# Kernel optimization log

Hardware: AMD Instinct MI355X
Metric: run time of the kernel (lower is better)

## Reference

```python
import jax, jax.numpy as jnp
import numpy as np

D_MODEL = 1024
NUM_HEADS = 16
D_FF = 4096
MAX_SEQ_LEN = 2048
THETA = 10000.0
EPS = 1e-5
B, S = 2, 2048


def setup_inputs() -> dict:
    key = jax.random.key(0)
    ks = jax.random.split(key, 10)
    scale = 0.02
    inp = {
        "in_features": jax.random.normal(ks[0], (B, S, D_MODEL), dtype=jnp.float32),
        "token_positions": jnp.broadcast_to(jnp.arange(S, dtype=jnp.int32), (B, S)),
        "q_w": jax.random.normal(ks[1], (D_MODEL, D_MODEL), dtype=jnp.float32) * scale,
        "k_w": jax.random.normal(ks[2], (D_MODEL, D_MODEL), dtype=jnp.float32) * scale,
        "v_w": jax.random.normal(ks[3], (D_MODEL, D_MODEL), dtype=jnp.float32) * scale,
        "o_w": jax.random.normal(ks[4], (D_MODEL, D_MODEL), dtype=jnp.float32) * scale,
        "ln1_w": jnp.ones((D_MODEL,), dtype=jnp.float32),
        "ln2_w": jnp.ones((D_MODEL,), dtype=jnp.float32),
        "ffn_w1": jax.random.normal(ks[5], (D_FF, D_MODEL), dtype=jnp.float32) * scale,
        "ffn_w2": jax.random.normal(ks[6], (D_MODEL, D_FF), dtype=jnp.float32) * scale,
        "ffn_w3": jax.random.normal(ks[7], (D_FF, D_MODEL), dtype=jnp.float32) * scale,
    }
    return inp


def _rmsnorm(x, w, eps=EPS):
    return x * jax.lax.rsqrt(jnp.mean(x * x, axis=-1, keepdims=True) + eps) * w


def _rope(x, pos, theta=THETA):
    # x: [B, H, S, Dh]; pos: [B, S] int
    dh = x.shape[-1]
    inv_freq = theta ** (-jnp.arange(0, dh, 2, dtype=jnp.float32) / dh)  # [Dh/2]
    ang = pos.astype(jnp.float32)[..., None] * inv_freq                  # [B, S, Dh/2]
    cos = jnp.cos(ang)[:, None, :, :]  # [B, 1, S, Dh/2]
    sin = jnp.sin(ang)[:, None, :, :]
    x1, x2 = x[..., 0::2], x[..., 1::2]
    r1 = x1 * cos - x2 * sin
    r2 = x1 * sin + x2 * cos
    return jnp.stack([r1, r2], axis=-1).reshape(x.shape)


def _block(x, pos, q_w, k_w, v_w, o_w, ln1_w, ln2_w, w1, w2, w3):
    b, s, d = x.shape
    h, dh = NUM_HEADS, d // NUM_HEADS
    # Pre-LN attention
    xn = _rmsnorm(x, ln1_w)
    q = jnp.einsum('bsd,ed->bse', xn, q_w).reshape(b, s, h, dh).transpose(0, 2, 1, 3)
    k = jnp.einsum('bsd,ed->bse', xn, k_w).reshape(b, s, h, dh).transpose(0, 2, 1, 3)
    v = jnp.einsum('bsd,ed->bse', xn, v_w).reshape(b, s, h, dh).transpose(0, 2, 1, 3)
    q = _rope(q, pos)
    k = _rope(k, pos)
    scores = jnp.einsum('bhqd,bhkd->bhqk', q, k) / jnp.sqrt(jnp.float32(dh))
    causal = jnp.tril(jnp.ones((s, s), dtype=bool))
    scores = jnp.where(causal, scores, jnp.float32(-1e9))
    attn = jax.nn.softmax(scores, axis=-1)
    ctx = jnp.einsum('bhqk,bhkd->bhqd', attn, v).transpose(0, 2, 1, 3).reshape(b, s, d)
    attn_out = jnp.einsum('bsd,ed->bse', ctx, o_w)
    x = x + attn_out
    # Pre-LN SwiGLU FFN
    xn2 = _rmsnorm(x, ln2_w)
    g = jnp.einsum('bsd,fd->bsf', xn2, w1)
    u = jnp.einsum('bsd,fd->bsf', xn2, w3)
    ffn_out = jnp.einsum('bsf,df->bsd', jax.nn.silu(g) * u, w2)
    return x + ffn_out


def reference(in_features, token_positions, q_w, k_w, v_w, o_w, ln1_w, ln2_w, ffn_w1, ffn_w2, ffn_w3):
    return _block(in_features, token_positions, q_w, k_w, v_w, o_w, ln1_w, ln2_w, ffn_w1, ffn_w2, ffn_w3)
```

## Files before the change

### kernel.cpp

```cpp
#include <hip/hip_runtime.h>
#include <hip/hip_bf16.h>

typedef __attribute__((ext_vector_type(8))) __bf16 bf16x8;
typedef __attribute__((ext_vector_type(4))) float f32x4;

#define DEV static __device__ __forceinline__

DEV unsigned short f2bf(float f) {
  __bf16 h = (__bf16)f;
  union { __bf16 h; unsigned short u; } v; v.h = h;
  return v.u;
}
DEV float bf2f(unsigned short h) {
  union { unsigned int u; float f; } v; v.u = ((unsigned int)h) << 16;
  return v.f;
}
DEV f32x4 mfma16(bf16x8 a, bf16x8 b, f32x4 c) {
  return __builtin_amdgcn_mfma_f32_16x16x32_bf16(a, b, c, 0, 0, 0);
}
DEV void gload_lds16(const void* g, void* l) {
  __builtin_amdgcn_global_load_lds((__attribute__((address_space(1))) void*)g,
                                   (__attribute__((address_space(3))) void*)l,
                                   16, 0, 0);
}
#if __has_builtin(__builtin_amdgcn_exp2f)
DEV float fexp2(float x) { return __builtin_amdgcn_exp2f(x); }
#else
DEV float fexp2(float x) { return exp2f(x); }
#endif

struct CvtArgs { const float* src[7]; int cum[8]; };
__global__ __launch_bounds__(256) void cvt_all(CvtArgs a, unsigned short* __restrict__ dst) {
  int i = (blockIdx.x * 256 + threadIdx.x) * 4;
  if (i >= a.cum[7]) return;
  int w = 0;
#pragma unroll 7
  for (int t = 0; t < 7; ++t) if (i >= a.cum[t + 1]) w = t + 1;
  float4 v = *(const float4*)(a.src[w] + (i - a.cum[w]));
  dst[i + 0] = f2bf(v.x);
  dst[i + 1] = f2bf(v.y);
  dst[i + 2] = f2bf(v.z);
  dst[i + 3] = f2bf(v.w);
}

__global__ __launch_bounds__(256) void rmsnorm_k(const float* __restrict__ x,
                                                 const float* __restrict__ w,
                                                 unsigned short* __restrict__ out) {
  int row = blockIdx.x;
  int tid = threadIdx.x;
  const float* xr = x + (size_t)row * 1024;
  float4 v = *(const float4*)(xr + tid * 4);
  float ss = v.x * v.x + v.y * v.y + v.z * v.z + v.w * v.w;
#pragma unroll
  for (int m = 32; m >= 1; m >>= 1) ss += __shfl_xor(ss, m);
  __shared__ float red[4];
  int wid = tid >> 6;
  if ((tid & 63) == 0) red[wid] = ss;
  __syncthreads();
  float tot = red[0] + red[1] + red[2] + red[3];
  float rs = rsqrtf(tot * (1.0f / 1024.0f) + 1e-5f);
  float4 wv = *(const float4*)(w + tid * 4);
  unsigned short* o = out + (size_t)row * 1024 + tid * 4;
  o[0] = f2bf(v.x * rs * wv.x);
  o[1] = f2bf(v.y * rs * wv.y);
  o[2] = f2bf(v.z * rs * wv.z);
  o[3] = f2bf(v.w * rs * wv.w);
}

__global__ __launch_bounds__(256) void rope2_k(unsigned short* __restrict__ q,
                                               unsigned short* __restrict__ k,
                                               const int* __restrict__ pos) {
  int gid = blockIdx.x * 256 + threadIdx.x;
  unsigned short* x = (gid < 2097152) ? q : k;
  int idx = gid & 2097151;
  int i = idx & 31;
  int s = (idx >> 5) & 2047;
  int bh = idx >> 16;
  int b = bh >> 4;
  float p = (float)pos[b * 2048 + s];
  float inv = exp2f(-(float)i * 0.4152410118609203f);
  float ang = p * inv;
  float sn = sinf(ang), cs = cosf(ang);
  size_t base = (((size_t)bh * 2048) + s) * 64 + 2 * i;
  float x1 = bf2f(x[base]), x2 = bf2f(x[base + 1]);
  x[base]     = f2bf(x1 * cs - x2 * sn);
  x[base + 1] = f2bf(x1 * sn + x2 * cs);
}

template <int MODE>
DEV void gemm8_body(const unsigned short* __restrict__ A, int lda,
                    const unsigned short* __restrict__ B, int ldb,
                    int bm, int bn, int kbase, int nt,
                    unsigned short* __restrict__ outb, float* __restrict__ outf,
                    const float* __restrict__ resid, const unsigned short* __restrict__ gate,
                    unsigned short* As, unsigned short* Bs) {
  const int tid = threadIdx.x;
  const int lane = tid & 63, wid = tid >> 6;
  const int wr = wid >> 2, wc = wid & 3;
  const int m0 = bm * 256, n0 = bn * 256;

  const int r0 = tid >> 2, r1 = 128 + (tid >> 2), cc = tid & 3;
  const int sc0 = (cc ^ ((r0 >> 1) & 3)) * 8;
  const int sc1 = (cc ^ ((r1 >> 1) & 3)) * 8;
  const size_t arow0 = (size_t)(m0 + r0) * lda, arow1 = (size_t)(m0 + r1) * lda;
  const size_t brow0 = (size_t)(n0 + r0) * ldb, brow1 = (size_t)(n0 + r1) * ldb;
  const int du0 = tid * 8, du1 = (512 + tid) * 8;

  auto stA = [&](int t, int kh) {
    unsigned short* d = As + ((((t & 1) << 1) | kh) * 8192);
    const unsigned short* s = A + kbase + t * 64 + kh * 32;
    gload_lds16(s + arow0 + sc0, d + du0);
    gload_lds16(s + arow1 + sc1, d + du1);
  };
  auto stB = [&](int t, int kh) {
    unsigned short* d = Bs + ((((t & 1) << 1) | kh) * 8192);
    const unsigned short* s = B + kbase + t * 64 + kh * 32;
    gload_lds16(s + brow0 + sc0, d + du0);
    gload_lds16(s + brow1 + sc1, d + du1);
  };

  const int fcol = ((lane >> 4) ^ ((lane >> 1) & 3)) * 8;
  const int frow = lane & 15;
  const int abase = (wr * 128 + frow) * 32 + fcol;
  const int bbase = (wc * 64 + frow) * 32 + fcol;

  f32x4 acc[8][4] = {};
  bf16x8 a[4], b[4];

#define LOADA(buf, ks, mh) { const unsigned short* p_ = As + (((buf) << 1) | (ks)) * 8192 + abase + (mh) * 2048; \
  a[0] = *(const bf16x8*)(p_); a[1] = *(const bf16x8*)(p_ + 512); \
  a[2] = *(const bf16x8*)(p_ + 1024); a[3] = *(const bf16x8*)(p_ + 1536); }
#define LOADB(buf, ks) { const unsigned short* p_ = Bs + (((buf) << 1) | (ks)) * 8192 + bbase; \
  b[0] = *(const bf16x8*)(p_); b[1] = *(const bf16x8*)(p_ + 512); \
  b[2] = *(const bf16x8*)(p_ + 1024); b[3] = *(const bf16x8*)(p_ + 1536); }
#define MFMAQ(mh) { _Pragma("unroll") for (int fi = 0; fi < 4; ++fi) \
  _Pragma("unroll") for (int j = 0; j < 4; ++j) \
    acc[(mh) * 4 + fi][j] = mfma16(a[fi], b[j], acc[(mh) * 4 + fi][j]); }
#define LGK0() { asm volatile("s_waitcnt lgkmcnt(0)" ::: "memory"); __builtin_amdgcn_sched_barrier(0); }

  stA(0, 0); stB(0, 0); stA(0, 1); stB(0, 1);
  stA(1, 0); stB(1, 0);
  asm volatile("s_waitcnt vmcnt(4)" ::: "memory");
  __builtin_amdgcn_s_barrier();

  for (int t = 0; t < nt; ++t) {
    const int buf = t & 1;
    LOADA(buf, 0, 0); LOADB(buf, 0);
    if (t + 1 < nt) stA(t + 1, 1);
    __builtin_amdgcn_s_barrier();
    LGK0();
    __builtin_amdgcn_s_setprio(1); MFMAQ(0); __builtin_amdgcn_s_setprio(0);
    __builtin_amdgcn_s_barrier();
    LOADA(buf, 0, 1);
    if (t + 1 < nt) stB(t + 1, 1);
    __builtin_amdgcn_s_barrier();
    LGK0();
    __builtin_amdgcn_s_setprio(1); MFMAQ(1); __builtin_amdgcn_s_setprio(0);
    __builtin_amdgcn_s_barrier();
    LOADA(buf, 1, 0); LOADB(buf, 1);
    if (t + 2 < nt) stA(t + 2, 0);
    __builtin_amdgcn_s_barrier();
    LGK0();
    __builtin_amdgcn_s_setprio(1); MFMAQ(0); __builtin_amdgcn_s_setprio(0);
    __builtin_amdgcn_s_barrier();
    LOADA(buf, 1, 1);
    if (t + 2 < nt) stB(t + 2, 0);
    __builtin_amdgcn_s_barrier();
    LGK0();
    __builtin_amdgcn_s_setprio(1); MFMAQ(1); __builtin_amdgcn_s_setprio(0);
    if (t + 1 < nt) {
      if (t + 2 < nt) { asm volatile("s_waitcnt vmcnt(4)" ::: "memory"); }
      else            { asm volatile("s_waitcnt vmcnt(0)" ::: "memory"); }
      __builtin_amdgcn_s_barrier();
    }
  }
#undef LOADA
#undef LOADB
#undef MFMAQ
#undef LGK0

#pragma unroll
  for (int i = 0; i < 8; ++i)
#pragma unroll
    for (int j = 0; j < 4; ++j)
#pragma unroll
      for (int r = 0; r < 4; ++r) {
        int m = m0 + wr * 128 + i * 16 + ((lane >> 4) << 2) + r;
        int n = n0 + wc * 64 + j * 16 + (lane & 15);
        float v = acc[i][j][r];
        if (MODE == 0) {
          unsigned short* dst = outb + ((n >= 1024) ? 4194304 : 0);
          int nn = n & 1023;
          int bb = m >> 11, s = m & 2047, hh = nn >> 6, dd = nn & 63;
          dst[(((size_t)bb * 16 + hh) * 2048 + s) * 64 + dd] = f2bf(v);
        } else if (MODE == 1) {
          int hh = m >> 6, dd = m & 63, bb = n >> 11, s = n & 2047;
          outb[(((size_t)bb * 16 + hh) * 64 + dd) * 2048 + s] = f2bf(v);
        } else if (MODE == 2) {
          size_t idx = (size_t)m * 1024 + n;
          outf[idx] = resid[idx] + v;
        } else if (MODE == 3) {
          outb[(size_t)m * 4096 + n] = f2bf(v);
        } else if (MODE == 4) {
          size_t idx = (size_t)m * 4096 + n;
          float g = bf2f(gate[idx]);
          outb[idx] = f2bf(g / (1.0f + __expf(-g)) * v);
        } else {
          outf[(size_t)m * 1024 + n] = v;
        }
      }
}

DEV void swz_map(int bid, int nwg, int MT, int& bm, int& bn) {
  int cpx = nwg >> 3;
  int sw = (bid & 7) * cpx + (bid >> 3);
  bm = sw % MT;
  bn = sw / MT;
}

template <int MODE>
__global__ __launch_bounds__(512, 2) void gemm8_k(const unsigned short* __restrict__ A, int lda,
                                                  const unsigned short* __restrict__ B, int ldb,
                                                  int MT, int kz, int nt,
                                                  unsigned short* __restrict__ outb,
                                                  float* __restrict__ outf,
                                                  const float* __restrict__ resid,
                                                  const unsigned short* __restrict__ gate) {
  __shared__ __align__(16) unsigned short lds[65536];
  int bm, bn;
  swz_map(blockIdx.x, gridDim.x, MT, bm, bn);
  int kb = kz * blockIdx.y;
  float* of = outf;
  if (MODE == 5) of += (size_t)blockIdx.y * 4194304;
  gemm8_body<MODE>(A, lda, B, ldb, bm, bn, kb, nt, outb, of, resid, gate, lds, lds + 32768);
}

__global__ __launch_bounds__(512, 2) void gemm8_qkv(const unsigned short* __restrict__ xn,
                                                    const unsigned short* __restrict__ wqk,
                                                    const unsigned short* __restrict__ wv,
                                                    unsigned short* __restrict__ qk_out,
                                                    unsigned short* __restrict__ vt_out) {
  __shared__ __align__(16) unsigned short lds[65536];
  int bid = blockIdx.x;
  if (bid < 128) {
    int bm, bn;
    swz_map(bid, 128, 16, bm, bn);
    gemm8_body<0>(xn, 1024, wqk, 1024, bm, bn, 0, 16, qk_out, nullptr, nullptr, nullptr, lds, lds + 32768);
  } else {
    bid -= 128;
    int bm, bn;
    swz_map(bid, 64, 4, bm, bn);
    gemm8_body<1>(wv, 1024, xn, 1024, bm, bn, 0, 16, vt_out, nullptr, nullptr, nullptr, lds, lds + 32768);
  }
}

__global__ __launch_bounds__(256) void gemm_wo(const unsigned short* __restrict__ A,
                                               const unsigned short* __restrict__ Bw,
                                               float* __restrict__ outf,
                                               const float* __restrict__ resid) {
  __shared__ __align__(16) unsigned short As[128 * 64];
  __shared__ __align__(16) unsigned short Bs[128 * 64];
  const int K = 1024, N = 1024;
  const int tid = threadIdx.x;
  const int wid = tid >> 6, lane = tid & 63;
  const int wr = wid >> 1, wc = wid & 1;
  const int m0 = blockIdx.x * 128, n0 = blockIdx.y * 128;
  const int sw = (lane & 7) * 8;
  f32x4 acc[4][4] = {};

  for (int k0 = 0; k0 < K; k0 += 64) {
    __syncthreads();
#pragma unroll
    for (int it = 0; it < 4; ++it) {
      int c = wid * 4 + it;
      int row = c * 8 + (lane >> 3);
      int col = ((lane & 7) ^ (row & 7)) * 8;
      gload_lds16(A + (size_t)(m0 + row) * K + k0 + col, As + c * 512);
      gload_lds16(Bw + (size_t)(n0 + row) * K + k0 + col, Bs + c * 512);
    }
    asm volatile("s_waitcnt vmcnt(0)" ::: "memory");
    __syncthreads();
#pragma unroll
    for (int kk = 0; kk < 2; ++kk) {
      const int kof = (kk * 32 + (lane >> 4) * 8) ^ sw;
      bf16x8 af[4], bfr[4];
#pragma unroll
      for (int i = 0; i < 4; ++i) {
        af[i]  = *(const bf16x8*)(As + (wr * 64 + i * 16 + (lane & 15)) * 64 + kof);
        bfr[i] = *(const bf16x8*)(Bs + (wc * 64 + i * 16 + (lane & 15)) * 64 + kof);
      }
#pragma unroll
      for (int i = 0; i < 4; ++i)
#pragma unroll
        for (int j = 0; j < 4; ++j) acc[i][j] = mfma16(af[i], bfr[j], acc[i][j]);
    }
  }
  const int rb = m0 + wr * 64 + ((lane >> 4) * 4);
  const int cb = n0 + wc * 64 + (lane & 15);
#pragma unroll
  for (int i = 0; i < 4; ++i)
#pragma unroll
    for (int r = 0; r < 4; ++r) {
      int m = rb + i * 16 + r;
#pragma unroll
      for (int j = 0; j < 4; ++j) {
        size_t idx = (size_t)m * N + cb + j * 16;
        outf[idx] = resid[idx] + acc[i][j][r];
      }
    }
}

__global__ __launch_bounds__(256) void reduce_k(float* __restrict__ out,
                                                const float* __restrict__ part) {
  int i = (blockIdx.x * 256 + threadIdx.x) * 4;
  float4 o = *(const float4*)(out + i);
  float4 p0 = *(const float4*)(part + i);
  float4 p1 = *(const float4*)(part + 4194304 + i);
  float4 p2 = *(const float4*)(part + 8388608 + i);
  float4 p3 = *(const float4*)(part + 12582912 + i);
  o.x += p0.x + p1.x + p2.x + p3.x;
  o.y += p0.y + p1.y + p2.y + p3.y;
  o.z += p0.z + p1.z + p2.z + p3.z;
  o.w += p0.w + p1.w + p2.w + p3.w;
  *(float4*)(out + i) = o;
}

__global__ __launch_bounds__(256) void attn_k(const unsigned short* __restrict__ q,
                                              const unsigned short* __restrict__ k,
                                              const unsigned short* __restrict__ vt,
                                              unsigned short* __restrict__ ctx) {
  __shared__ __align__(16) unsigned short Ks[2][64 * 64];
  __shared__ __align__(16) unsigned short Vs[2][64 * 64];
  __shared__ __align__(16) unsigned short Ps[4][16 * 64];
  const int bid = blockIdx.x;
  const int bh = (bid & 7) * 4 + ((bid >> 3) & 3);
  const int qt = 31 - (bid >> 5);
  const int tid = threadIdx.x, wid = tid >> 6, lane = tid & 63;
  const size_t bhS = (size_t)bh * 2048;
  const size_t bhD = (size_t)bh * 64 * 2048;
  const int b = bh >> 4, hh = bh & 15;
  const int sw = (lane & 7) * 8;
  const float SC2 = 0.18033688011112042f;

  const int c0 = wid * 2, c1 = wid * 2 + 1;
  const int row0 = c0 * 8 + (lane >> 3), row1 = c1 * 8 + (lane >> 3);
  const int col0 = ((lane & 7) ^ (row0 & 7)) * 8;
  const int col1 = ((lane & 7) ^ (row1 & 7)) * 8;

  auto stage = [&](int kt, int buf) {
    gload_lds16(k + (bhS + kt * 64 + row0) * 64 + col0, &Ks[buf][c0 * 512]);
    gload_lds16(k + (bhS + kt * 64 + row1) * 64 + col1, &Ks[buf][c1 * 512]);
    gload_lds16(vt + bhD + (size_t)row0 * 2048 + kt * 64 + col0, &Vs[buf][c0 * 512]);
    gload_lds16(vt + bhD + (size_t)row1 * 2048 + kt * 64 + col1, &Vs[buf][c1 * 512]);
  };

  const int q0 = qt * 64;
  bf16x8 qf[2];
  {
    const unsigned short* qp = q + (bhS + q0 + wid * 16 + (lane & 15)) * 64 + (lane >> 4) * 8;
    qf[0] = *(const bf16x8*)qp;
    qf[1] = *(const bf16x8*)(qp + 32);
#pragma unroll
    for (int jj = 0; jj < 8; ++jj) {
      qf[0][jj] = (__bf16)((float)qf[0][jj] * SC2);
      qf[1][jj] = (__bf16)((float)qf[1][jj] * SC2);
    }
  }
  float mrow[4], lrow[4];
  f32x4 o[4] = {};
#pragma unroll
  for (int r = 0; r < 4; ++r) { mrow[r] = -1e30f; lrow[r] = 0.0f; }
  const int rowb = q0 + wid * 16 + ((lane >> 4) * 4);

  stage(0, 0);
  if (qt > 0) { stage(1, 1); asm volatile("s_waitcnt vmcnt(4)" ::: "memory"); }
  else        {              asm volatile("s_waitcnt vmcnt(0)" ::: "memory"); }
  __builtin_amdgcn_s_barrier();

  for (int kt = 0; kt <= qt; ++kt) {
    const int cur = kt & 1;
    f32x4 s[4];
#pragma unroll
    for (int nt = 0; nt < 4; ++nt) {
      f32x4 z = {};
#pragma unroll
      for (int ks = 0; ks < 2; ++ks) {
        int kof = (ks * 32 + (lane >> 4) * 8) ^ sw;
        bf16x8 kf = *(const bf16x8*)(&Ks[cur][(nt * 16 + (lane & 15)) * 64 + kof]);
        z = mfma16(qf[ks], kf, z);
      }
      s[nt] = z;
    }
    const bool diag = (kt == qt);
    float pm[4];
    bool ok = true;
#pragma unroll
    for (int r = 0; r < 4; ++r) {
      float mx = -3e38f;
#pragma unroll
      for (int nt = 0; nt < 4; ++nt) {
        float val = s[nt][r];
        if (diag && (kt * 64 + nt * 16 + (lane & 15)) > (rowb + r)) val = -3e38f;
        s[nt][r] = val;
        mx = fmaxf(mx, val);
      }
      mx = fmaxf(mx, __shfl_xor(mx, 1));
      mx = fmaxf(mx, __shfl_xor(mx, 2));
      mx = fmaxf(mx, __shfl_xor(mx, 4));
      mx = fmaxf(mx, __shfl_xor(mx, 8));
      pm[r] = mx;
      ok = ok && (mx <= mrow[r] + 11.5f);
    }
    if (!__all(ok)) {
#pragma unroll
      for (int r = 0; r < 4; ++r) {
        float mn = fmaxf(mrow[r], pm[r]);
        float al = fexp2(mrow[r] - mn);
        lrow[r] *= al;
#pragma unroll
        for (int d = 0; d < 4; ++d) o[d][r] *= al;
        mrow[r] = mn;
      }
    }
#pragma unroll
    for (int r = 0; r < 4; ++r) {
      float sum = 0.0f;
#pragma unroll
      for (int nt = 0; nt < 4; ++nt) {
        float pv = fexp2(s[nt][r] - mrow[r]);
        s[nt][r] = pv;
        sum += pv;
      }
      lrow[r] += sum;
    }
#pragma unroll
    for (int nt = 0; nt < 4; ++nt)
#pragma unroll
      for (int r = 0; r < 4; ++r) {
        int qr = (lane >> 4) * 4 + r;
        Ps[wid][qr * 64 + ((nt * 16 + (lane & 15)) ^ ((qr & 7) * 8))] = f2bf(s[nt][r]);
      }
#pragma unroll
    for (int ks = 0; ks < 2; ++ks) {
      int qr2 = lane & 15;
      bf16x8 pf = *(const bf16x8*)(&Ps[wid][qr2 * 64 + ((ks * 32 + (lane >> 4) * 8) ^ ((qr2 & 7) * 8))]);
      int kof = (ks * 32 + (lane >> 4) * 8) ^ sw;
#pragma unroll
      for (int d = 0; d < 4; ++d) {
        bf16x8 vf = *(const bf16x8*)(&Vs[cur][(d * 16 + (lane & 15)) * 64 + kof]);
        o[d] = mfma16(pf, vf, o[d]);
      }
    }
    __builtin_amdgcn_s_barrier();
    if (kt + 2 <= qt) {
      stage(kt + 2, cur);
      asm volatile("s_waitcnt vmcnt(4)" ::: "memory");
    } else if (kt + 1 <= qt) {
      asm volatile("s_waitcnt vmcnt(0)" ::: "memory");
    }
    __builtin_amdgcn_s_barrier();
  }
#pragma unroll
  for (int r = 0; r < 4; ++r) {
    lrow[r] += __shfl_xor(lrow[r], 1);
    lrow[r] += __shfl_xor(lrow[r], 2);
    lrow[r] += __shfl_xor(lrow[r], 4);
    lrow[r] += __shfl_xor(lrow[r], 8);
  }
#pragma unroll
  for (int d = 0; d < 4; ++d)
#pragma unroll
    for (int r = 0; r < 4; ++r) {
      float val = o[d][r] / lrow[r];
      ctx[((size_t)b * 2048 + (rowb + r)) * 1024 + hh * 64 + d * 16 + (lane & 15)] = f2bf(val);
    }
}

extern "C" void kernel_launch(void* const* d_in, const int* in_sizes, int n_in,
                              void* d_out, int out_size, void* d_ws, size_t ws_size,
                              hipStream_t stream) {
  (void)in_sizes; (void)n_in; (void)out_size; (void)ws_size;
  const float* in_f = (const float*)d_in[0];
  const int* pos    = (const int*)d_in[1];
  const float* q_w  = (const float*)d_in[2];
  const float* k_w  = (const float*)d_in[3];
  const float* v_w  = (const float*)d_in[4];
  const float* o_w  = (const float*)d_in[5];
  const float* ln1  = (const float*)d_in[6];
  const float* ln2  = (const float*)d_in[7];
  const float* w1   = (const float*)d_in[8];
  const float* w2   = (const float*)d_in[9];
  const float* w3   = (const float*)d_in[10];
  float* out = (float*)d_out;

  unsigned short* ws = (unsigned short*)d_ws;
  unsigned short* wb   = ws;
  unsigned short* wqkb = wb;
  unsigned short* wvb  = wb + 2097152;
  unsigned short* wob  = wb + 3145728;
  unsigned short* w1b  = wb + 4194304;
  unsigned short* w2b  = wb + 8388608;
  unsigned short* w3b  = wb + 12582912;
  unsigned short* xn   = ws + 16777216;
  unsigned short* qb   = ws + 20971520;
  unsigned short* kb   = ws + 25165824;
  unsigned short* vb   = ws + 29360128;
  unsigned short* cx   = ws + 33554432;
  unsigned short* gb   = ws + 37748736;
  float* part          = (float*)(ws + 20971520);
  unsigned short* hb   = ws + 54525952;

  CvtArgs ca;
  ca.src[0] = q_w; ca.src[1] = k_w; ca.src[2] = v_w; ca.src[3] = o_w;
  ca.src[4] = w1;  ca.src[5] = w2;  ca.src[6] = w3;
  ca.cum[0] = 0;        ca.cum[1] = 1048576;  ca.cum[2] = 2097152;  ca.cum[3] = 3145728;
  ca.cum[4] = 4194304;  ca.cum[5] = 8388608;  ca.cum[6] = 12582912; ca.cum[7] = 16777216;
  cvt_all<<<16384, 256, 0, stream>>>(ca, wb);

  rmsnorm_k<<<4096, 256, 0, stream>>>(in_f, ln1, xn);

  gemm8_qkv<<<192, 512, 0, stream>>>(xn, wqkb, wvb, qb, vb);

  rope2_k<<<16384, 256, 0, stream>>>(qb, kb, pos);

  attn_k<<<1024, 256, 0, stream>>>(qb, kb, vb, cx);

  gemm_wo<<<dim3(32, 8), 256, 0, stream>>>(cx, wob, out, in_f);

  rmsnorm_k<<<4096, 256, 0, stream>>>(out, ln2, xn);

  gemm8_k<3><<<256, 512, 0, stream>>>(xn, 1024, w1b, 1024, 16, 0, 16, gb, nullptr, nullptr, nullptr);
  gemm8_k<4><<<256, 512, 0, stream>>>(xn, 1024, w3b, 1024, 16, 0, 16, hb, nullptr, nullptr, gb);
  gemm8_k<5><<<dim3(64, 4), 512, 0, stream>>>(hb, 4096, w2b, 4096, 16, 1024, 16, nullptr, part, nullptr, nullptr);

  reduce_k<<<4096, 256, 0, stream>>>(out, part);
}
```

Baseline: 294.4 us.

## Rewrite attention with 32x32 MFMA, 128-row query tiles and register-resident P

```diff
diff --git a/kernel.cpp b/kernel.cpp
--- a/kernel.cpp
+++ b/kernel.cpp
@@ -3,6 +3,7 @@
 
 typedef __attribute__((ext_vector_type(8))) __bf16 bf16x8;
 typedef __attribute__((ext_vector_type(4))) float f32x4;
+typedef __attribute__((ext_vector_type(16))) float f32x16;
 
 #define DEV static __device__ __forceinline__
 
@@ -15,19 +16,23 @@
   union { unsigned int u; float f; } v; v.u = ((unsigned int)h) << 16;
   return v.f;
 }
+DEV unsigned pkbf(float lo, float hi) {
+  union { __bf16 h[2]; unsigned u; } v;
+  v.h[0] = (__bf16)lo; v.h[1] = (__bf16)hi;
+  return v.u;
+}
 DEV f32x4 mfma16(bf16x8 a, bf16x8 b, f32x4 c) {
   return __builtin_amdgcn_mfma_f32_16x16x32_bf16(a, b, c, 0, 0, 0);
+}
+DEV f32x16 mfma32(bf16x8 a, bf16x8 b, f32x16 c) {
+  return __builtin_amdgcn_mfma_f32_32x32x16_bf16(a, b, c, 0, 0, 0);
 }
 DEV void gload_lds16(const void* g, void* l) {
   __builtin_amdgcn_global_load_lds((__attribute__((address_space(1))) void*)g,
                                    (__attribute__((address_space(3))) void*)l,
                                    16, 0, 0);
 }
-#if __has_builtin(__builtin_amdgcn_exp2f)
-DEV float fexp2(float x) { return __builtin_amdgcn_exp2f(x); }
-#else
 DEV float fexp2(float x) { return exp2f(x); }
-#endif
 
 struct CvtArgs { const float* src[7]; int cum[8]; };
 __global__ __launch_bounds__(256) void cvt_all(CvtArgs a, unsigned short* __restrict__ dst) {
@@ -329,151 +334,142 @@
                                               const unsigned short* __restrict__ k,
                                               const unsigned short* __restrict__ vt,
                                               unsigned short* __restrict__ ctx) {
-  __shared__ __align__(16) unsigned short Ks[2][64 * 64];
-  __shared__ __align__(16) unsigned short Vs[2][64 * 64];
-  __shared__ __align__(16) unsigned short Ps[4][16 * 64];
+  __shared__ __align__(16) unsigned short Ks[2][4096];
+  __shared__ __align__(16) unsigned short Vs[2][4096];
   const int bid = blockIdx.x;
   const int bh = (bid & 7) * 4 + ((bid >> 3) & 3);
-  const int qt = 31 - (bid >> 5);
+  const int qtile = 15 - (bid >> 5);
   const int tid = threadIdx.x, wid = tid >> 6, lane = tid & 63;
+  const int l31 = lane & 31, hi = lane >> 5;
   const size_t bhS = (size_t)bh * 2048;
   const size_t bhD = (size_t)bh * 64 * 2048;
   const int b = bh >> 4, hh = bh & 15;
-  const int sw = (lane & 7) * 8;
   const float SC2 = 0.18033688011112042f;
 
-  const int c0 = wid * 2, c1 = wid * 2 + 1;
-  const int row0 = c0 * 8 + (lane >> 3), row1 = c1 * 8 + (lane >> 3);
-  const int col0 = ((lane & 7) ^ (row0 & 7)) * 8;
-  const int col1 = ((lane & 7) ^ (row1 & 7)) * 8;
+  const int c0 = wid * 2, c1 = c0 + 1;
+  const int rl0 = c0 * 4 + (lane >> 4), rl1 = c1 * 4 + (lane >> 4);
+  const int u0 = ((lane & 15) ^ (rl0 & 15)) * 8;
+  const int u1 = ((lane & 15) ^ (rl1 & 15)) * 8;
+  const int sr0 = rl0 + ((u0 >> 6) << 5), scol0 = u0 & 63;
+  const int sr1 = rl1 + ((u1 >> 6) << 5), scol1 = u1 & 63;
 
   auto stage = [&](int kt, int buf) {
-    gload_lds16(k + (bhS + kt * 64 + row0) * 64 + col0, &Ks[buf][c0 * 512]);
-    gload_lds16(k + (bhS + kt * 64 + row1) * 64 + col1, &Ks[buf][c1 * 512]);
-    gload_lds16(vt + bhD + (size_t)row0 * 2048 + kt * 64 + col0, &Vs[buf][c0 * 512]);
-    gload_lds16(vt + bhD + (size_t)row1 * 2048 + kt * 64 + col1, &Vs[buf][c1 * 512]);
+    gload_lds16(k + (bhS + kt * 64 + sr0) * 64 + scol0, &Ks[buf][c0 * 512]);
+    gload_lds16(k + (bhS + kt * 64 + sr1) * 64 + scol1, &Ks[buf][c1 * 512]);
+    gload_lds16(vt + bhD + (size_t)sr0 * 2048 + kt * 64 + scol0, &Vs[buf][c0 * 512]);
+    gload_lds16(vt + bhD + (size_t)sr1 * 2048 + kt * 64 + scol1, &Vs[buf][c1 * 512]);
   };
 
-  const int q0 = qt * 64;
-  bf16x8 qf[2];
+  const int qrow = qtile * 128 + wid * 32 + l31;
+  bf16x8 qf[4];
   {
-    const unsigned short* qp = q + (bhS + q0 + wid * 16 + (lane & 15)) * 64 + (lane >> 4) * 8;
-    qf[0] = *(const bf16x8*)qp;
-    qf[1] = *(const bf16x8*)(qp + 32);
-#pragma unroll
-    for (int jj = 0; jj < 8; ++jj) {
-      qf[0][jj] = (__bf16)((float)qf[0][jj] * SC2);
-      qf[1][jj] = (__bf16)((float)qf[1][jj] * SC2);
+    const unsigned short* qp = q + (bhS + qrow) * 64 + hi * 8;
+#pragma unroll
+    for (int c = 0; c < 4; ++c) {
+      bf16x8 t = *(const bf16x8*)(qp + c * 16);
+#pragma unroll
+      for (int j = 0; j < 8; ++j) t[j] = (__bf16)((float)t[j] * SC2);
+      qf[c] = t;
     }
   }
-  float mrow[4], lrow[4];
-  f32x4 o[4] = {};
-#pragma unroll
-  for (int r = 0; r < 4; ++r) { mrow[r] = -1e30f; lrow[r] = 0.0f; }
-  const int rowb = q0 + wid * 16 + ((lane >> 4) * 4);
+
+  float mrow = -1e30f, lrow = 0.0f;
+  f32x16 o0 = {}, o1 = {};
+  const int qw0 = qtile * 128 + wid * 32;
+  const int ktmax = (qw0 + 31) >> 6;
+  const int KT = 2 * qtile + 2;
+  const int rsw = (l31 & 15) * 8;
 
   stage(0, 0);
-  if (qt > 0) { stage(1, 1); asm volatile("s_waitcnt vmcnt(4)" ::: "memory"); }
-  else        {              asm volatile("s_waitcnt vmcnt(0)" ::: "memory"); }
+  stage(1, 1);
+  asm volatile("s_waitcnt vmcnt(4)" ::: "memory");
   __builtin_amdgcn_s_barrier();
 
-  for (int kt = 0; kt <= qt; ++kt) {
+  for (int kt = 0; kt < KT; ++kt) {
     const int cur = kt & 1;
-    f32x4 s[4];
-#pragma unroll
-    for (int nt = 0; nt < 4; ++nt) {
-      f32x4 z = {};
-#pragma unroll
-      for (int ks = 0; ks < 2; ++ks) {
-        int kof = (ks * 32 + (lane >> 4) * 8) ^ sw;
-        bf16x8 kf = *(const bf16x8*)(&Ks[cur][(nt * 16 + (lane & 15)) * 64 + kof]);
-        z = mfma16(qf[ks], kf, z);
-      }
-      s[nt] = z;
-    }
-    const bool diag = (kt == qt);
-    float pm[4];
-    bool ok = true;
-#pragma unroll
-    for (int r = 0; r < 4; ++r) {
-      float mx = -3e38f;
-#pragma unroll
-      for (int nt = 0; nt < 4; ++nt) {
-        float val = s[nt][r];
-        if (diag && (kt * 64 + nt * 16 + (lane & 15)) > (rowb + r)) val = -3e38f;
-        s[nt][r] = val;
-        mx = fmaxf(mx, val);
-      }
-      mx = fmaxf(mx, __shfl_xor(mx, 1));
-      mx = fmaxf(mx, __shfl_xor(mx, 2));
-      mx = fmaxf(mx, __shfl_xor(mx, 4));
-      mx = fmaxf(mx, __shfl_xor(mx, 8));
-      pm[r] = mx;
-      ok = ok && (mx <= mrow[r] + 11.5f);
-    }
-    if (!__all(ok)) {
-#pragma unroll
-      for (int r = 0; r < 4; ++r) {
-        float mn = fmaxf(mrow[r], pm[r]);
-        float al = fexp2(mrow[r] - mn);
-        lrow[r] *= al;
-#pragma unroll
-        for (int d = 0; d < 4; ++d) o[d][r] *= al;
-        mrow[r] = mn;
-      }
-    }
-#pragma unroll
-    for (int r = 0; r < 4; ++r) {
+    if (kt <= ktmax) {
+      f32x16 sa0 = {}, sa1 = {};
+#pragma unroll
+      for (int c = 0; c < 4; ++c) {
+        int colbase = c * 16 + hi * 8;
+        bf16x8 k0 = *(const bf16x8*)(&Ks[cur][l31 * 128 + (colbase ^ rsw)]);
+        bf16x8 k1 = *(const bf16x8*)(&Ks[cur][l31 * 128 + ((64 + colbase) ^ rsw)]);
+        sa0 = mfma32(k0, qf[c], sa0);
+        sa1 = mfma32(k1, qf[c], sa1);
+      }
+      float s[32];
+#pragma unroll
+      for (int r = 0; r < 16; ++r) { s[r] = sa0[r]; s[16 + r] = sa1[r]; }
+      if (kt * 64 + 63 > qw0) {
+        const int qg = qw0 + l31;
+#pragma unroll
+        for (int r = 0; r < 16; ++r) {
+          int key0 = kt * 64 + (r & 3) + 8 * (r >> 2) + 4 * hi;
+          if (key0 > qg) s[r] = -3e38f;
+          if (key0 + 32 > qg) s[16 + r] = -3e38f;
+        }
+      }
+      float pmax = s[0];
+#pragma unroll
+      for (int r = 1; r < 32; ++r) pmax = fmaxf(pmax, s[r]);
+      pmax = fmaxf(pmax, __shfl_xor(pmax, 32));
+      if (!__all(pmax <= mrow + 11.5f)) {
+        float mnew = fmaxf(mrow, pmax);
+        float dl = mrow - mnew;
+        mrow = mnew;
+        lrow *= fexp2(dl);
+#pragma unroll
+        for (int r = 0; r < 16; ++r) {
+          int qsrc = (r & 3) + 8 * (r >> 2) + 4 * hi;
+          float ar = fexp2(__shfl(dl, qsrc, 64));
+          o0[r] *= ar; o1[r] *= ar;
+        }
+      }
       float sum = 0.0f;
 #pragma unroll
-      for (int nt = 0; nt < 4; ++nt) {
-        float pv = fexp2(s[nt][r] - mrow[r]);
-        s[nt][r] = pv;
-        sum += pv;
-      }
-      lrow[r] += sum;
-    }
-#pragma unroll
-    for (int nt = 0; nt < 4; ++nt)
-#pragma unroll
-      for (int r = 0; r < 4; ++r) {
-        int qr = (lane >> 4) * 4 + r;
-        Ps[wid][qr * 64 + ((nt * 16 + (lane & 15)) ^ ((qr & 7) * 8))] = f2bf(s[nt][r]);
-      }
-#pragma unroll
-    for (int ks = 0; ks < 2; ++ks) {
-      int qr2 = lane & 15;
-      bf16x8 pf = *(const bf16x8*)(&Ps[wid][qr2 * 64 + ((ks * 32 + (lane >> 4) * 8) ^ ((qr2 & 7) * 8))]);
-      int kof = (ks * 32 + (lane >> 4) * 8) ^ sw;
-#pragma unroll
-      for (int d = 0; d < 4; ++d) {
-        bf16x8 vf = *(const bf16x8*)(&Vs[cur][(d * 16 + (lane & 15)) * 64 + kof]);
-        o[d] = mfma16(pf, vf, o[d]);
-      }
-    }
-    __builtin_amdgcn_s_barrier();
-    if (kt + 2 <= qt) {
+      for (int r = 0; r < 32; ++r) { s[r] = fexp2(s[r] - mrow); sum += s[r]; }
+      lrow += sum;
+      unsigned pw[16];
+#pragma unroll
+      for (int i = 0; i < 16; ++i) pw[i] = pkbf(s[2 * i], s[2 * i + 1]);
+#pragma unroll
+      for (int g = 0; g < 4; ++g) {
+        asm volatile("v_permlane32_swap_b32 %0, %1" : "+v"(pw[4 * g]), "+v"(pw[4 * g + 2]));
+        asm volatile("v_permlane32_swap_b32 %0, %1" : "+v"(pw[4 * g + 1]), "+v"(pw[4 * g + 3]));
+      }
+#pragma unroll
+      for (int g = 0; g < 4; ++g) {
+        union { unsigned w[4]; bf16x8 v; } pa;
+        pa.w[0] = pw[4 * g]; pa.w[1] = pw[4 * g + 1];
+        pa.w[2] = pw[4 * g + 2]; pa.w[3] = pw[4 * g + 3];
+        int kl = g * 16 + hi * 8;
+        bf16x8 v0 = *(const bf16x8*)(&Vs[cur][l31 * 128 + (kl ^ rsw)]);
+        bf16x8 v1 = *(const bf16x8*)(&Vs[cur][l31 * 128 + ((64 + kl) ^ rsw)]);
+        o0 = mfma32(pa.v, v0, o0);
+        o1 = mfma32(pa.v, v1, o1);
+      }
+    }
+    __builtin_amdgcn_s_barrier();
+    if (kt + 2 < KT) {
       stage(kt + 2, cur);
       asm volatile("s_waitcnt vmcnt(4)" ::: "memory");
-    } else if (kt + 1 <= qt) {
+    } else if (kt + 1 < KT) {
       asm volatile("s_waitcnt vmcnt(0)" ::: "memory");
     }
     __builtin_amdgcn_s_barrier();
   }
-#pragma unroll
-  for (int r = 0; r < 4; ++r) {
-    lrow[r] += __shfl_xor(lrow[r], 1);
-    lrow[r] += __shfl_xor(lrow[r], 2);
-    lrow[r] += __shfl_xor(lrow[r], 4);
-    lrow[r] += __shfl_xor(lrow[r], 8);
+
+  lrow += __shfl_xor(lrow, 32);
+  float inv = 1.0f / lrow;
+#pragma unroll
+  for (int r = 0; r < 16; ++r) {
+    int qsrc = (r & 3) + 8 * (r >> 2) + 4 * hi;
+    float li = __shfl(inv, qsrc, 64);
+    int srow = qtile * 128 + wid * 32 + qsrc;
+    size_t base = ((size_t)b * 2048 + srow) * 1024 + hh * 64 + l31;
+    ctx[base]      = f2bf(o0[r] * li);
+    ctx[base + 32] = f2bf(o1[r] * li);
   }
-#pragma unroll
-  for (int d = 0; d < 4; ++d)
-#pragma unroll
-    for (int r = 0; r < 4; ++r) {
-      float val = o[d][r] / lrow[r];
-      ctx[((size_t)b * 2048 + (rowb + r)) * 1024 + hh * 64 + d * 16 + (lane & 15)] = f2bf(val);
-    }
 }
 
 extern "C" void kernel_launch(void* const* d_in, const int* in_sizes, int n_in,
@@ -523,7 +519,7 @@
 
   rope2_k<<<16384, 256, 0, stream>>>(qb, kb, pos);
 
-  attn_k<<<1024, 256, 0, stream>>>(qb, kb, vb, cx);
+  attn_k<<<512, 256, 0, stream>>>(qb, kb, vb, cx);
 
   gemm_wo<<<dim3(32, 8), 256, 0, stream>>>(cx, wob, out, in_f);
 
```

Measured after the change: 302.0 us. +2.6%, slower.
